# Kernel tuning notes

Measured on AMD Instinct MI355X. Metric: run time of the kernel, lower is better.

Reference implementation:

```python
import jax, jax.numpy as jnp
import numpy as np

N, T, C = 100000, 12, 32  # nodes, periods, hidden (A3TGCN out_channels hardcoded 32)
E = 3_200_000


def setup_inputs() -> dict:
    key = jax.random.key(0)
    ks = jax.random.split(key, 20)
    s_g = 1.0 / np.sqrt(1.0)        # GCNConv glorot-ish for in=1
    s_l = 1.0 / np.sqrt(2.0 * C)    # torch Linear default for in=2C
    s_h = 1.0 / np.sqrt(C)
    u = lambda k, shape, s: jax.random.uniform(k, shape, jnp.float32, -s, s)
    return {
        "x": jax.random.normal(ks[0], (N, T), jnp.float32),
        "edge_index": jax.random.randint(ks[1], (2, E), 0, N, jnp.int32),
        "edge_weight": jax.random.uniform(ks[2], (E,), jnp.float32),
        # TGCN gate GCNConv params (in_channels=1, out=C)
        "w_z": u(ks[3], (1, C), s_g), "b_z": jnp.zeros((C,), jnp.float32),
        "w_r": u(ks[4], (1, C), s_g), "b_r": jnp.zeros((C,), jnp.float32),
        "w_h": u(ks[5], (1, C), s_g), "b_h": jnp.zeros((C,), jnp.float32),
        # TGCN gate Linear params (torch layout [out=C, in=2C])
        "lw_z": u(ks[6], (C, 2 * C), s_l), "lb_z": u(ks[7], (C,), s_l),
        "lw_r": u(ks[8], (C, 2 * C), s_l), "lb_r": u(ks[9], (C,), s_l),
        "lw_h": u(ks[10], (C, 2 * C), s_l), "lb_h": u(ks[11], (C,), s_l),
        # A3TGCN temporal attention
        "att": jax.random.uniform(ks[12], (T,), jnp.float32),
        # head Linear(32, 1)
        "head_w": u(ks[13], (1, C), s_h), "head_b": u(ks[14], (1,), s_h),
    }


def reference(x, edge_index, edge_weight, w_z, b_z, w_r, b_r, w_h, b_h,
              lw_z, lb_z, lw_r, lb_r, lw_h, lb_h, att, head_w, head_b):
    n = x.shape[0]
    # --- GCN normalization with self-loops (fill value 1) ---
    loop = jnp.arange(n)
    s = jnp.concatenate([edge_index[0], loop])
    d = jnp.concatenate([edge_index[1], loop])
    w = jnp.concatenate([edge_weight, jnp.ones((n,), edge_weight.dtype)])
    deg = jax.ops.segment_sum(w, d, num_segments=n)
    dinv = jnp.where(deg > 0, jax.lax.rsqrt(deg), 0.0)
    norm = dinv[s] * w * dinv[d]
    # --- shared sparse aggregation: A_hat @ X for all periods at once ---
    # in_channels = 1, so GCNConv(X_t) = (A_hat x_t) * W + b; aggregate scalars [N,T]
    agg = jax.ops.segment_sum(norm[:, None] * x[s], d, num_segments=n)  # [N, T]
    # gate convolutions, [N, T, C]
    cz = agg[:, :, None] * w_z[0] + b_z
    ch = agg[:, :, None] * w_h[0] + b_h
    # A3TGCN passes H=None every period -> hidden starts at 0 each step, so
    # linear([conv, H]) reduces to conv @ W[:, :C].T + b, and the reset gate R
    # multiplies H=0 (no effect on output).
    Z = jax.nn.sigmoid(jnp.einsum('ntc,oc->nto', cz, lw_z[:, :C]) + lb_z)
    Ht = jnp.tanh(jnp.einsum('ntc,oc->nto', ch, lw_h[:, :C]) + lb_h)
    Hp = (1.0 - Z) * Ht  # per-period hidden state, [N, T, C]
    probs = jax.nn.softmax(att)
    h = jnp.einsum('t,ntc->nc', probs, Hp)  # attention-weighted temporal sum
    h = jax.nn.relu(h)
    return h @ head_w.T + head_b  # [N, 1]
```

## Files before the change

### kernel.cpp

```cpp
#include <hip/hip_runtime.h>

#define N_NODES 100000
#define T_P 12
#define C_H 32
#define E_EDGES 3200000

#define NODES_PER_B 128
#define NB 782
#define MAX_BE 4608

#define VEC_E (E_EDGES / 4)
#define P1_THREADS 512
#define P1_VECS 1024
#define EPB 4096
#define NBLK1 ((VEC_E + P1_VECS - 1) / P1_VECS)


__global__ void params_kernel(const float* __restrict__ wz, const float* __restrict__ bz,
                              const float* __restrict__ wh, const float* __restrict__ bh,
                              const float* __restrict__ lwz, const float* __restrict__ lbz,
                              const float* __restrict__ lwh, const float* __restrict__ lbh,
                              const float* __restrict__ att, float* __restrict__ P,
                              int* __restrict__ cursor) {
    int o = threadIdx.x;
    if (o < NB) cursor[o] = 0;
    if (o < C_H) {
        float az = 0.f, bzv = 0.f, ah = 0.f, bhv = 0.f;
        for (int c = 0; c < C_H; ++c) {
            float lz = lwz[o * 2 * C_H + c];
            float lh = lwh[o * 2 * C_H + c];
            az += wz[c] * lz;  bzv += bz[c] * lz;
            ah += wh[c] * lh;  bhv += bh[c] * lh;
        }
        P[16 + o]  = az;  P[48 + o]  = bzv + lbz[o];
        P[80 + o]  = ah;  P[112 + o] = bhv + lbh[o];
    }
    if (o == 0) {
        float m = -1e30f;
        for (int t = 0; t < T_P; ++t) m = fmaxf(m, att[t]);
        float e[T_P], s = 0.f;
        for (int t = 0; t < T_P; ++t) { e[t] = __expf(att[t] - m); s += e[t]; }
        float inv = 1.0f / s;
        for (int t = 0; t < T_P; ++t) P[t] = e[t] * inv;
    }
}

__global__ void __launch_bounds__(512)
bucket_scatter_kernel(const int* __restrict__ src, const int* __restrict__ dst,
                      const float* __restrict__ w, int* __restrict__ cursor,
                      float2* __restrict__ entries) {
    __shared__ float2 stage[EPB];
    __shared__ unsigned short bina[EPB];
    __shared__ unsigned short sidx[EPB];
    __shared__ int h[NB];
    __shared__ int scanb[1024];
    __shared__ int claim[NB];
    int tid = threadIdx.x;
    int vbase = blockIdx.x * P1_VECS;
    int ne = E_EDGES - vbase * 4;
    if (ne > EPB) ne = EPB;
    for (int i = tid; i < NB; i += 512) h[i] = 0;
    __syncthreads();
    const int4* d4 = (const int4*)dst;
    const int4* s4 = (const int4*)src;
    const float4* w4 = (const float4*)w;
    int rra[8];
    int valid[2];
#pragma unroll
    for (int half = 0; half < 2; ++half) {
        int v = vbase + half * 512 + tid;
        valid[half] = (v < VEC_E);
        if (valid[half]) {
            int4 d = d4[v];
            int4 s = s4[v];
            float4 ww = w4[v];
            int kb = half * 2048 + tid;
            int bin, dl;
            bin = d.x >> 7; dl = d.x & 127;
            rra[half * 4 + 0] = atomicAdd(&h[bin], 1);
            stage[kb] = make_float2(__int_as_float(s.x | (dl << 17)), ww.x);
            bina[kb] = (unsigned short)bin;
            bin = d.y >> 7; dl = d.y & 127;
            rra[half * 4 + 1] = atomicAdd(&h[bin], 1);
            stage[kb + 512] = make_float2(__int_as_float(s.y | (dl << 17)), ww.y);
            bina[kb + 512] = (unsigned short)bin;
            bin = d.z >> 7; dl = d.z & 127;
            rra[half * 4 + 2] = atomicAdd(&h[bin], 1);
            stage[kb + 1024] = make_float2(__int_as_float(s.z | (dl << 17)), ww.z);
            bina[kb + 1024] = (unsigned short)bin;
            bin = d.w >> 7; dl = d.w & 127;
            rra[half * 4 + 3] = atomicAdd(&h[bin], 1);
            stage[kb + 1536] = make_float2(__int_as_float(s.w | (dl << 17)), ww.w);
            bina[kb + 1536] = (unsigned short)bin;
        }
    }
    __syncthreads();
    scanb[tid]       = (tid < NB) ? h[tid] : 0;
    scanb[tid + 512] = (tid + 512 < NB) ? h[tid + 512] : 0;
    __syncthreads();
    for (int d = 1; d < 1024; d <<= 1) {
        int t0 = (tid >= d) ? scanb[tid - d] : 0;
        int t1 = (tid + 512 >= d) ? scanb[tid + 512 - d] : 0;
        __syncthreads();
        scanb[tid] += t0;
        scanb[tid + 512] += t1;
        __syncthreads();
    }
    for (int i = tid; i < NB; i += 512) {
        int c = h[i];
        claim[i] = c ? atomicAdd(&cursor[i], c) : 0;
    }
#pragma unroll
    for (int half = 0; half < 2; ++half) {
        if (valid[half]) {
            int kb = half * 2048 + tid;
#pragma unroll
            for (int j = 0; j < 4; ++j) {
                int k = kb + j * 512;
                int b = bina[k];
                sidx[scanb[b] - h[b] + rra[half * 4 + j]] = (unsigned short)k;
            }
        }
    }
    __syncthreads();
    for (int p = tid; p < ne; p += 512) {
        int k = sidx[p];
        float2 e = stage[k];
        int b = bina[k];
        int pos = claim[b] + (p - (scanb[b] - h[b]));
        if (pos < MAX_BE) entries[b * MAX_BE + pos] = e;
    }
}

__global__ void __launch_bounds__(512)
prep_kernel(const float2* __restrict__ entries, const int* __restrict__ cursor,
            const float* __restrict__ x, float* __restrict__ dinv, float* __restrict__ y) {
    __shared__ float wsum[NODES_PER_B];
    __shared__ float dloc[NODES_PER_B];
    int tid = threadIdx.x;
    int b = blockIdx.x;
    int nbase = b << 7;
    int lo = b * MAX_BE;
    int ne = cursor[b]; if (ne > MAX_BE) ne = MAX_BE;
    if (tid < NODES_PER_B) wsum[tid] = 0.f;
    __syncthreads();
    for (int k = tid; k < ne; k += 512) {
        float2 e = entries[lo + k];
        atomicAdd(&wsum[(__float_as_int(e.x) >> 17) & 127], e.y);
    }
    __syncthreads();
    if (tid < NODES_PER_B) {
        int n = nbase + tid;
        float di = (n < N_NODES) ? rsqrtf(1.0f + wsum[tid]) : 0.f;
        dloc[tid] = di;
        if (n < N_NODES) dinv[n] = di;
    }
    __syncthreads();
    if (tid < 384) {
        int nl = tid / 3, q = tid - nl * 3;
        int n = nbase + nl;
        if (n < N_NODES) {
            float4 v = ((const float4*)x)[(size_t)n * 3 + q];
            float di = dloc[nl];
            v.x *= di; v.y *= di; v.z *= di; v.w *= di;
            ((float4*)y)[((size_t)n << 2) + q] = v;
        }
    }
    if (tid < NODES_PER_B) {
        int n = nbase + tid;
        if (n < N_NODES) ((float4*)y)[((size_t)n << 2) + 3] = make_float4(0.f, 0.f, 0.f, 0.f);
    }
}

__global__ void __launch_bounds__(512)
sort_gather_kernel(const float2* __restrict__ entries, const int* __restrict__ cursor,
                   const float* __restrict__ dinv, const float* __restrict__ y,
                   const float* __restrict__ P, const float* __restrict__ head_w,
                   const float* __restrict__ head_b, float* __restrict__ out) {
    __shared__ float2 stage[MAX_BE];
    __shared__ unsigned short sidx[MAX_BE];
    __shared__ int   cnt[NODES_PER_B];
    __shared__ int   inc[NODES_PER_B];
    __shared__ int   rnk[NODES_PER_B];
    __shared__ float Ps[160];
    __shared__ float hws[C_H];
    int tid = threadIdx.x;
    int b = blockIdx.x;
    int lo = b * MAX_BE;
    int ne = cursor[b]; if (ne > MAX_BE) ne = MAX_BE;
    if (tid < 160) Ps[tid] = P[tid];
    if (tid < C_H) hws[tid] = head_w[tid];
    if (tid < NODES_PER_B) cnt[tid] = 0;
    __syncthreads();
    for (int k = tid; k < ne; k += 512) {
        float2 e = entries[lo + k];
        stage[k] = e;
        atomicAdd(&cnt[(__float_as_int(e.x) >> 17) & 127], 1);
    }
    __syncthreads();
    if (tid < NODES_PER_B) inc[tid] = cnt[tid];
    __syncthreads();
    for (int d = 1; d < NODES_PER_B; d <<= 1) {
        int t = (tid >= d && tid < NODES_PER_B) ? inc[tid - d] : 0;
        __syncthreads();
        if (tid < NODES_PER_B) inc[tid] += t;
        __syncthreads();
    }
    if (tid < NODES_PER_B) rnk[tid] = inc[tid] - cnt[tid];
    __syncthreads();
    for (int k = tid; k < ne; k += 512) {
        int dl = (__float_as_int(stage[k].x) >> 17) & 127;
        int r = atomicAdd(&rnk[dl], 1);
        sidx[r] = (unsigned short)k;
    }
    __syncthreads();
    int nl = tid >> 2, lane = tid & 3;
    int n = (b << 7) + nl;
    if (n >= N_NODES) return;
    int end = inc[nl];
    int start = end - cnt[nl];
    const float4* yn = (const float4*)(y + ((size_t)n << 4));
    float4 a0 = make_float4(0.f, 0.f, 0.f, 0.f);
    float4 a1 = a0, a2 = a0;
    if (lane == 0)      a0 = yn[0];
    else if (lane == 1) a1 = yn[1];
    else if (lane == 2) a2 = yn[2];
    for (int j = start + lane; j < end; j += 4) {
        float2 ent = stage[sidx[j]];
        int s = __float_as_int(ent.x) & 0x1FFFF;
        float c = ent.y;
        const float4* ys = (const float4*)(y + ((size_t)s << 4));
        float4 s0 = ys[0], s1 = ys[1], s2 = ys[2];
        a0.x += c * s0.x; a0.y += c * s0.y; a0.z += c * s0.z; a0.w += c * s0.w;
        a1.x += c * s1.x; a1.y += c * s1.y; a1.z += c * s1.z; a1.w += c * s1.w;
        a2.x += c * s2.x; a2.y += c * s2.y; a2.z += c * s2.z; a2.w += c * s2.w;
    }
#define RED4(v) v += __shfl_xor(v, 1); v += __shfl_xor(v, 2)
    RED4(a0.x); RED4(a0.y); RED4(a0.z); RED4(a0.w);
    RED4(a1.x); RED4(a1.y); RED4(a1.z); RED4(a1.w);
    RED4(a2.x); RED4(a2.y); RED4(a2.z); RED4(a2.w);
#undef RED4
    float din = dinv[n];
    float av[T_P];
    av[0] = a0.x * din; av[1] = a0.y * din; av[2]  = a0.z * din; av[3]  = a0.w * din;
    av[4] = a1.x * din; av[5] = a1.y * din; av[6]  = a1.z * din; av[7]  = a1.w * din;
    av[8] = a2.x * din; av[9] = a2.y * din; av[10] = a2.z * din; av[11] = a2.w * din;
    float acc = 0.f;
#pragma unroll
    for (int k = 0; k < 8; ++k) {
        int c = (lane << 3) + k;
        float Az = Ps[16 + c], Bz = Ps[48 + c], Ah = Ps[80 + c], Bh = Ps[112 + c];
        float hc = 0.f;
#pragma unroll
        for (int t = 0; t < T_P; ++t) {
            float a = av[t];
            float oz = 1.f / (1.f + __expf(a * Az + Bz));
            float vv = a * Ah + Bh;
            float th = 1.f - 2.f / (1.f + __expf(2.f * vv));
            hc += Ps[t] * oz * th;
        }
        acc += fmaxf(hc, 0.f) * hws[c];
    }
    acc += __shfl_xor(acc, 1);
    acc += __shfl_xor(acc, 2);
    if (lane == 0) out[n] = acc + head_b[0];
}

extern "C" void kernel_launch(void* const* d_in, const int* in_sizes, int n_in,
                              void* d_out, int out_size, void* d_ws, size_t ws_size,
                              hipStream_t stream) {
    const float* x    = (const float*)d_in[0];
    const int*   ei   = (const int*)d_in[1];
    const float* ew   = (const float*)d_in[2];
    const float* w_z  = (const float*)d_in[3];
    const float* b_z  = (const float*)d_in[4];
    const float* w_h  = (const float*)d_in[7];
    const float* b_h  = (const float*)d_in[8];
    const float* lw_z = (const float*)d_in[9];
    const float* lb_z = (const float*)d_in[10];
    const float* lw_h = (const float*)d_in[13];
    const float* lb_h = (const float*)d_in[14];
    const float* att  = (const float*)d_in[15];
    const float* hw   = (const float*)d_in[16];
    const float* hb   = (const float*)d_in[17];
    float* out = (float*)d_out;

    float* wsf      = (float*)d_ws;
    float* P        = wsf;
    float* dinv     = P + 256;
    int*   cursor   = (int*)(dinv + N_NODES);
    float* y        = wsf + 101040;
    float2* entries = (float2*)(y + (size_t)N_NODES * 16);

    const int* srcp = ei;
    const int* dstp = ei + E_EDGES;

    params_kernel<<<1, 1024, 0, stream>>>(w_z, b_z, w_h, b_h, lw_z, lb_z, lw_h, lb_h,
                                          att, P, cursor);
    bucket_scatter_kernel<<<NBLK1, P1_THREADS, 0, stream>>>(srcp, dstp, ew, cursor, entries);
    prep_kernel<<<NB, 512, 0, stream>>>(entries, cursor, x, dinv, y);
    sort_gather_kernel<<<NB, 512, 0, stream>>>(entries, cursor, dinv, y, P, hw, hb, out);
}
```

Measured before the change: 243.4 us.

## Scatter edges directly to global buckets and sort in registers without index indirection

The bucket scatter kernel stops staging edges in shared memory and locally sorting them. It now does a histogram pass over dst, claims global cursor ranges, then re-reads src/dst/w and writes each edge straight to its bucket slot, with twice as many edges per block. The sort-gather kernel keeps up to 9 entries per thread in registers and places them directly into sorted order in shared memory, which removes the sidx indirection and a second atomic pass; it also adds an occupancy hint to the launch bounds. The trade-off is re-reading dst from global memory and writing scattered, uncoalesced entries in place of coalesced bucketed stores.

```diff
diff --git a/kernel.cpp b/kernel.cpp
--- a/kernel.cpp
+++ b/kernel.cpp
@@ -11,8 +11,7 @@
 
 #define VEC_E (E_EDGES / 4)
 #define P1_THREADS 512
-#define P1_VECS 1024
-#define EPB 4096
+#define P1_VECS 2048
 #define NBLK1 ((VEC_E + P1_VECS - 1) / P1_VECS)
 
 
@@ -49,86 +48,50 @@
 bucket_scatter_kernel(const int* __restrict__ src, const int* __restrict__ dst,
                       const float* __restrict__ w, int* __restrict__ cursor,
                       float2* __restrict__ entries) {
-    __shared__ float2 stage[EPB];
-    __shared__ unsigned short bina[EPB];
-    __shared__ unsigned short sidx[EPB];
     __shared__ int h[NB];
-    __shared__ int scanb[1024];
     __shared__ int claim[NB];
     int tid = threadIdx.x;
     int vbase = blockIdx.x * P1_VECS;
-    int ne = E_EDGES - vbase * 4;
-    if (ne > EPB) ne = EPB;
     for (int i = tid; i < NB; i += 512) h[i] = 0;
     __syncthreads();
     const int4* d4 = (const int4*)dst;
+    int rra[16];
+#pragma unroll
+    for (int q = 0; q < 4; ++q) {
+        int v = vbase + q * 512 + tid;
+        if (v < VEC_E) {
+            int4 d = d4[v];
+            rra[q * 4 + 0] = atomicAdd(&h[d.x >> 7], 1);
+            rra[q * 4 + 1] = atomicAdd(&h[d.y >> 7], 1);
+            rra[q * 4 + 2] = atomicAdd(&h[d.z >> 7], 1);
+            rra[q * 4 + 3] = atomicAdd(&h[d.w >> 7], 1);
+        }
+    }
+    __syncthreads();
+    for (int i = tid; i < NB; i += 512) {
+        int c = h[i];
+        claim[i] = c ? atomicAdd(&cursor[i], c) : 0;
+    }
+    __syncthreads();
     const int4* s4 = (const int4*)src;
     const float4* w4 = (const float4*)w;
-    int rra[8];
-    int valid[2];
-#pragma unroll
-    for (int half = 0; half < 2; ++half) {
-        int v = vbase + half * 512 + tid;
-        valid[half] = (v < VEC_E);
-        if (valid[half]) {
+#pragma unroll
+    for (int q = 0; q < 4; ++q) {
+        int v = vbase + q * 512 + tid;
+        if (v < VEC_E) {
             int4 d = d4[v];
             int4 s = s4[v];
             float4 ww = w4[v];
-            int kb = half * 2048 + tid;
-            int bin, dl;
-            bin = d.x >> 7; dl = d.x & 127;
-            rra[half * 4 + 0] = atomicAdd(&h[bin], 1);
-            stage[kb] = make_float2(__int_as_float(s.x | (dl << 17)), ww.x);
-            bina[kb] = (unsigned short)bin;
-            bin = d.y >> 7; dl = d.y & 127;
-            rra[half * 4 + 1] = atomicAdd(&h[bin], 1);
-            stage[kb + 512] = make_float2(__int_as_float(s.y | (dl << 17)), ww.y);
-            bina[kb + 512] = (unsigned short)bin;
-            bin = d.z >> 7; dl = d.z & 127;
-            rra[half * 4 + 2] = atomicAdd(&h[bin], 1);
-            stage[kb + 1024] = make_float2(__int_as_float(s.z | (dl << 17)), ww.z);
-            bina[kb + 1024] = (unsigned short)bin;
-            bin = d.w >> 7; dl = d.w & 127;
-            rra[half * 4 + 3] = atomicAdd(&h[bin], 1);
-            stage[kb + 1536] = make_float2(__int_as_float(s.w | (dl << 17)), ww.w);
-            bina[kb + 1536] = (unsigned short)bin;
-        }
-    }
-    __syncthreads();
-    scanb[tid]       = (tid < NB) ? h[tid] : 0;
-    scanb[tid + 512] = (tid + 512 < NB) ? h[tid + 512] : 0;
-    __syncthreads();
-    for (int d = 1; d < 1024; d <<= 1) {
-        int t0 = (tid >= d) ? scanb[tid - d] : 0;
-        int t1 = (tid + 512 >= d) ? scanb[tid + 512 - d] : 0;
-        __syncthreads();
-        scanb[tid] += t0;
-        scanb[tid + 512] += t1;
-        __syncthreads();
-    }
-    for (int i = tid; i < NB; i += 512) {
-        int c = h[i];
-        claim[i] = c ? atomicAdd(&cursor[i], c) : 0;
-    }
-#pragma unroll
-    for (int half = 0; half < 2; ++half) {
-        if (valid[half]) {
-            int kb = half * 2048 + tid;
-#pragma unroll
-            for (int j = 0; j < 4; ++j) {
-                int k = kb + j * 512;
-                int b = bina[k];
-                sidx[scanb[b] - h[b] + rra[half * 4 + j]] = (unsigned short)k;
-            }
-        }
-    }
-    __syncthreads();
-    for (int p = tid; p < ne; p += 512) {
-        int k = sidx[p];
-        float2 e = stage[k];
-        int b = bina[k];
-        int pos = claim[b] + (p - (scanb[b] - h[b]));
-        if (pos < MAX_BE) entries[b * MAX_BE + pos] = e;
+            int bin, dl, pos;
+            bin = d.x >> 7; dl = d.x & 127; pos = claim[bin] + rra[q * 4 + 0];
+            if (pos < MAX_BE) entries[bin * MAX_BE + pos] = make_float2(__int_as_float(s.x | (dl << 17)), ww.x);
+            bin = d.y >> 7; dl = d.y & 127; pos = claim[bin] + rra[q * 4 + 1];
+            if (pos < MAX_BE) entries[bin * MAX_BE + pos] = make_float2(__int_as_float(s.y | (dl << 17)), ww.y);
+            bin = d.z >> 7; dl = d.z & 127; pos = claim[bin] + rra[q * 4 + 2];
+            if (pos < MAX_BE) entries[bin * MAX_BE + pos] = make_float2(__int_as_float(s.z | (dl << 17)), ww.z);
+            bin = d.w >> 7; dl = d.w & 127; pos = claim[bin] + rra[q * 4 + 3];
+            if (pos < MAX_BE) entries[bin * MAX_BE + pos] = make_float2(__int_as_float(s.w | (dl << 17)), ww.w);
+        }
     }
 }
 
@@ -172,16 +135,14 @@
     }
 }
 
-__global__ void __launch_bounds__(512)
+__global__ void __launch_bounds__(512, 8)
 sort_gather_kernel(const float2* __restrict__ entries, const int* __restrict__ cursor,
                    const float* __restrict__ dinv, const float* __restrict__ y,
                    const float* __restrict__ P, const float* __restrict__ head_w,
                    const float* __restrict__ head_b, float* __restrict__ out) {
     __shared__ float2 stage[MAX_BE];
-    __shared__ unsigned short sidx[MAX_BE];
     __shared__ int   cnt[NODES_PER_B];
     __shared__ int   inc[NODES_PER_B];
-    __shared__ int   rnk[NODES_PER_B];
     __shared__ float Ps[160];
     __shared__ float hws[C_H];
     int tid = threadIdx.x;
@@ -192,10 +153,16 @@
     if (tid < C_H) hws[tid] = head_w[tid];
     if (tid < NODES_PER_B) cnt[tid] = 0;
     __syncthreads();
-    for (int k = tid; k < ne; k += 512) {
-        float2 e = entries[lo + k];
-        stage[k] = e;
-        atomicAdd(&cnt[(__float_as_int(e.x) >> 17) & 127], 1);
+    float2 ent[9];
+    int    rr[9];
+#pragma unroll
+    for (int i = 0; i < 9; ++i) {
+        int k = tid + i * 512;
+        if (k < ne) {
+            float2 e = entries[lo + k];
+            ent[i] = e;
+            rr[i] = atomicAdd(&cnt[(__float_as_int(e.x) >> 17) & 127], 1);
+        }
     }
     __syncthreads();
     if (tid < NODES_PER_B) inc[tid] = cnt[tid];
@@ -206,12 +173,13 @@
         if (tid < NODES_PER_B) inc[tid] += t;
         __syncthreads();
     }
-    if (tid < NODES_PER_B) rnk[tid] = inc[tid] - cnt[tid];
-    __syncthreads();
-    for (int k = tid; k < ne; k += 512) {
-        int dl = (__float_as_int(stage[k].x) >> 17) & 127;
-        int r = atomicAdd(&rnk[dl], 1);
-        sidx[r] = (unsigned short)k;
+#pragma unroll
+    for (int i = 0; i < 9; ++i) {
+        int k = tid + i * 512;
+        if (k < ne) {
+            int dl = (__float_as_int(ent[i].x) >> 17) & 127;
+            stage[inc[dl] - cnt[dl] + rr[i]] = ent[i];
+        }
     }
     __syncthreads();
     int nl = tid >> 2, lane = tid & 3;
@@ -226,9 +194,9 @@
     else if (lane == 1) a1 = yn[1];
     else if (lane == 2) a2 = yn[2];
     for (int j = start + lane; j < end; j += 4) {
-        float2 ent = stage[sidx[j]];
-        int s = __float_as_int(ent.x) & 0x1FFFF;
-        float c = ent.y;
+        float2 e = stage[j];
+        int s = __float_as_int(e.x) & 0x1FFFF;
+        float c = e.y;
         const float4* ys = (const float4*)(y + ((size_t)s << 4));
         float4 s0 = ys[0], s1 = ys[1], s2 = ys[2];
         a0.x += c * s0.x; a0.y += c * s0.y; a0.z += c * s0.z; a0.w += c * s0.w;
```

Result: no change. 243.1 us (-0.1%).
